# Performance work log

Measured on AMD Instinct MI355X. Metric: run time of the kernel, lower is better.

The kernel has to match this reference:

```python
import jax, jax.numpy as jnp
import numpy as np

D = 512      # d_model
H = 8        # n_heads
HD = D // H  # head_dim
WIN = 128    # local window
CB = 8       # chunk base
NL = 3       # hierarchy levels
DFF = 1536
B, S = 4, 4096
EPS = 1e-6


def setup_inputs() -> dict:
    key = jax.random.key(0)
    ks = jax.random.split(key, 12)
    sd = 0.02
    inp = {
        'x': jax.random.normal(ks[0], (B, S, D), jnp.float32),
        'norm1_w': jnp.ones((D,), jnp.float32),
        'norm2_w': jnp.ones((D,), jnp.float32),
        'wq': jax.random.normal(ks[1], (D, D), jnp.float32) * sd,
        'wk': jax.random.normal(ks[2], (D, D), jnp.float32) * sd,
        'wv': jax.random.normal(ks[3], (D, D), jnp.float32) * sd,
        'wo': jax.random.normal(ks[4], (D, D), jnp.float32) * sd,
        'gamma': jnp.full((NL,), 0.1, jnp.float32),
        'w1': jax.random.normal(ks[5], (D, DFF), jnp.float32) * sd,
        'w2': jax.random.normal(ks[6], (D, DFF), jnp.float32) * sd,
        'w3': jax.random.normal(ks[7], (DFF, D), jnp.float32) * sd,
    }
    return inp


def rmsnorm(x, w):
    return x * jax.lax.rsqrt(jnp.mean(x * x, axis=-1, keepdims=True) + EPS) * w


def hier_attn(x, wq, wk, wv, wo, gamma):
    b, s, _ = x.shape
    scale = HD ** -0.5
    q = (x @ wq).reshape(b, s, H, HD).transpose(0, 2, 1, 3)  # (b,H,s,hd)
    k = (x @ wk).reshape(b, s, H, HD).transpose(0, 2, 1, 3)
    v = (x @ wv).reshape(b, s, H, HD).transpose(0, 2, 1, 3)

    nb = s // WIN
    qb = q.reshape(b, H, nb, WIN, HD)
    kp = jnp.concatenate([jnp.zeros_like(k[:, :, :WIN]), k], axis=2).reshape(b, H, nb + 1, WIN, HD)
    vp = jnp.concatenate([jnp.zeros_like(v[:, :, :WIN]), v], axis=2).reshape(b, H, nb + 1, WIN, HD)
    kw = jnp.concatenate([kp[:, :, :-1], kp[:, :, 1:]], axis=3)  # (b,H,nb,2W,hd)
    vw = jnp.concatenate([vp[:, :, :-1], vp[:, :, 1:]], axis=3)
    sc = jnp.einsum('bhnqd,bhnkd->bhnqk', qb, kw) * scale
    a_ = jnp.arange(WIN)[:, None]
    j_ = jnp.arange(2 * WIN)[None, :]
    base = (j_ > a_) & (j_ <= a_ + WIN)
    blk = (jnp.arange(nb)[:, None, None] > 0) | (j_ >= WIN)  # first block has no left half
    mask = base[None] & blk                                  # (nb,W,2W)
    sc = jnp.where(mask[None, None], sc, -1e9)
    out = jnp.einsum('bhnqk,bhnkd->bhnqd', jax.nn.softmax(sc, axis=-1), vw).reshape(b, H, s, HD)

    # ---- levels 1..NL: causal attention over mean-pooled chunk summaries ----
    pos = jnp.arange(s)
    for lvl in range(1, NL + 1):
        C = CB ** lvl
        nc = s // C
        kc = k.reshape(b, H, nc, C, HD).mean(axis=3)
        vc = v.reshape(b, H, nc, C, HD).mean(axis=3)
        sl = jnp.einsum('bhsd,bhcd->bhsc', q, kc) * scale
        m = jnp.arange(nc)[None, :] < (pos // C)[:, None]    # chunk strictly in the past
        sl = jnp.where(m[None, None], sl, -1e9)
        p = jax.nn.softmax(sl, axis=-1)
        p = p * m.any(axis=-1)[None, None, :, None]          # zero rows with no valid chunk
        out = out + gamma[lvl - 1] * jnp.einsum('bhsc,bhcd->bhsd', p, vc)

    return out.transpose(0, 2, 1, 3).reshape(b, s, D) @ wo


def swiglu(x, w1, w2, w3):
    return (jax.nn.silu(x @ w1) * (x @ w2)) @ w3


def reference(x, norm1_w, norm2_w, wq, wk, wv, wo, gamma, w1, w2, w3):
    h = x + hier_attn(rmsnorm(x, norm1_w), wq, wk, wv, wo, gamma)
    return h + swiglu(rmsnorm(h, norm2_w), w1, w2, w3)
```

## Files before the change

### kernel.cpp

```cpp
#include <hip/hip_runtime.h>
#include <stdint.h>

typedef unsigned short US;
typedef __attribute__((ext_vector_type(8))) short short8;
typedef __attribute__((ext_vector_type(8))) US us8;
typedef __attribute__((ext_vector_type(4))) float f32x4;
typedef __attribute__((ext_vector_type(4))) int i32x4;

#define DEV static __device__ __forceinline__

DEV US f2b(float f){
  uint32_t u = __builtin_bit_cast(uint32_t, f);
  return (US)((u + 0x7fffu + ((u >> 16) & 1u)) >> 16);
}
DEV float b2f(US s){
  return __builtin_bit_cast(float, (uint32_t)((uint32_t)s << 16));
}
DEV short8 ldsfrag(const US* p){
  return __builtin_bit_cast(short8, *(const i32x4*)p);
}
DEV f32x4 MFMA(short8 a, short8 b, f32x4 c){
  return __builtin_amdgcn_mfma_f32_16x16x32_bf16(a, b, c, 0, 0, 0);
}
DEV void async16(const US* g, US* l){
  __builtin_amdgcn_global_load_lds(
      (const __attribute__((address_space(1))) unsigned int*)(const void*)g,
      (__attribute__((address_space(3))) unsigned int*)(void*)l,
      16, 0, 0);
}

struct WcvtArgs {
  const float* src[7];
  US* dst[7];
  int R[7];
  int C[7];
};

__global__ __launch_bounds__(256) void wcvt(WcvtArgs a){
  int z = blockIdx.z;
  int R = a.R[z], C = a.C[z];
  int tc = blockIdx.x*32, tr = blockIdx.y*32;
  if (tc >= C || tr >= R) return;
  __shared__ float T[32][33];
  int tx = threadIdx.x & 31, ty = threadIdx.x >> 5;
  const float* s = a.src[z];
  #pragma unroll
  for (int j=0;j<4;++j) T[ty + j*8][tx] = s[(size_t)(tr + ty + j*8)*C + tc + tx];
  __syncthreads();
  US* d = a.dst[z];
  #pragma unroll
  for (int j=0;j<4;++j) d[(size_t)(tc + ty + j*8)*R + tr + tx] = f2b(T[tx][ty + j*8]);
}

__global__ __launch_bounds__(256) void rmsnorm_k(const float* __restrict__ x,
                                                 const float* __restrict__ w,
                                                 US* __restrict__ o){
  int row = blockIdx.x*4 + (threadIdx.x >> 6);
  int l = threadIdx.x & 63;
  const float* xr = x + (size_t)row*512 + l*8;
  f32x4 a = *(const f32x4*)xr;
  f32x4 b = *(const f32x4*)(xr + 4);
  float ss = a[0]*a[0]+a[1]*a[1]+a[2]*a[2]+a[3]*a[3]
           + b[0]*b[0]+b[1]*b[1]+b[2]*b[2]+b[3]*b[3];
  #pragma unroll
  for (int mk=1; mk<64; mk<<=1) ss += __shfl_xor(ss, mk);
  float r = rsqrtf(ss*(1.0f/512.0f) + 1e-6f);
  const float* wr = w + l*8;
  f32x4 wa = *(const f32x4*)wr;
  f32x4 wb = *(const f32x4*)(wr + 4);
  us8 t;
  t[0]=f2b(a[0]*r*wa[0]); t[1]=f2b(a[1]*r*wa[1]);
  t[2]=f2b(a[2]*r*wa[2]); t[3]=f2b(a[3]*r*wa[3]);
  t[4]=f2b(b[0]*r*wb[0]); t[5]=f2b(b[1]*r*wb[1]);
  t[6]=f2b(b[2]*r*wb[2]); t[7]=f2b(b[3]*r*wb[3]);
  *(us8*)(o + (size_t)row*512 + l*8) = t;
}

template<int EPI>
__global__ __launch_bounds__(256) void gemm_bt(
    const US* __restrict__ A, const US* __restrict__ BT,
    int M, int N, int K,
    void* __restrict__ outp, const float* __restrict__ auxf,
    US* __restrict__ auxb)
{
  __shared__ __attribute__((aligned(16))) US As[128*64];
  __shared__ __attribute__((aligned(16))) US Bs[128*64];
  const int tid = threadIdx.x, l = tid & 63, w = tid >> 6;
  const int wr = w >> 1, wc = w & 1;
  const int gx = gridDim.x;
  int wg = blockIdx.y*gx + blockIdx.x;
  const int nwg = gx * gridDim.y;
  const int qq = nwg >> 3;
  wg = (wg & 7)*qq + (wg >> 3);
  const int m0 = (wg / gx)*128, n0 = (wg % gx)*128;
  (void)M;
  f32x4 acc[4][4] = {};
  for (int k0 = 0; k0 < K; k0 += 64){
    #pragma unroll
    for (int p=0;p<4;++p){
      int off  = p*4096 + w*1024 + l*16;
      int row  = off >> 7;
      int slot = (off >> 4) & 7;
      int ce   = ((slot ^ (row & 7)) << 3);
      async16(A  + (size_t)(m0 + row)*K + k0 + ce, As + p*2048 + w*512);
      async16(BT + (size_t)(n0 + row)*K + k0 + ce, Bs + p*2048 + w*512);
    }
    __syncthreads();
    short8 af[2][4], bg[2][4];
    #pragma unroll
    for (int kk=0;kk<2;++kk){
      const int sA = ((kk*4 + (l>>4)) ^ (l & 7)) << 3;
      #pragma unroll
      for (int i=0;i<4;++i){
        af[kk][i] = ldsfrag(&As[(wr*64 + i*16 + (l&15))*64 + sA]);
        bg[kk][i] = ldsfrag(&Bs[(wc*64 + i*16 + (l&15))*64 + sA]);
      }
    }
    #pragma unroll
    for (int kk=0;kk<2;++kk)
      #pragma unroll
      for (int i=0;i<4;++i)
        #pragma unroll
        for (int j=0;j<4;++j)
          acc[i][j] = MFMA(af[kk][i], bg[kk][j], acc[i][j]);
    __syncthreads();
  }
  #pragma unroll
  for (int i=0;i<4;++i)
    #pragma unroll
    for (int j=0;j<4;++j)
      #pragma unroll
      for (int r=0;r<4;++r){
        int m  = m0 + wr*64 + i*16 + (l>>4)*4 + r;
        int nn = n0 + wc*64 + j*16 + (l&15);
        float val = acc[i][j][r];
        if constexpr (EPI == 0){
          US* o = (US*)outp;
          int f = nn & 511, t = nn >> 9;
          size_t idx = (size_t)t*8388608
                     + ((size_t)(m>>12)*8 + (size_t)(f>>6))*262144
                     + (size_t)(m & 4095)*64 + (size_t)(f & 63);
          o[idx] = f2b(val);
        } else if constexpr (EPI == 1){
          float* o = (float*)outp;
          size_t idx = (size_t)m*N + nn;
          o[idx] = auxf[idx] + val;
        } else if constexpr (EPI == 2){
          US* o = (US*)outp;
          o[(size_t)m*N + nn] = f2b(val);
        } else if constexpr (EPI == 3){
          US* o = (US*)outp;
          size_t idx = (size_t)m*N + nn;
          float g = b2f(auxb[idx]);
          float sg = g / (1.f + __expf(-g));
          o[idx] = f2b(sg * val);
        } else {
          float* o = (float*)outp;
          size_t idx = (size_t)m*N + nn;
          o[idx] += val;
        }
      }
}

__global__ __launch_bounds__(256) void vtrans(const US* __restrict__ vin,
                                              US* __restrict__ vout){
  __shared__ US T[64*72];
  int s0 = blockIdx.x*64;
  int bh = blockIdx.y;
  int r = threadIdx.x >> 2, c0 = (threadIdx.x & 3)*16;
  const US* src = vin + ((size_t)bh*4096 + s0 + r)*64 + c0;
  *(i32x4*)&T[r*72 + c0]     = *(const i32x4*)src;
  *(i32x4*)&T[r*72 + c0 + 8] = *(const i32x4*)(src + 8);
  __syncthreads();
  int d = threadIdx.x >> 2, e0 = (threadIdx.x & 3)*16;
  US* dst = vout + ((size_t)bh*64 + d)*4096 + s0 + e0;
  us8 o0, o1;
  #pragma unroll
  for (int j=0;j<8;++j){ o0[j] = T[(e0+j)*72 + d]; o1[j] = T[(e0+8+j)*72 + d]; }
  *(us8*)dst = o0;
  *(us8*)(dst + 8) = o1;
}

__global__ __launch_bounds__(256) void poolkvt(
    const US* __restrict__ kin, US* __restrict__ kout,
    const US* __restrict__ vtin, US* __restrict__ vtout,
    int nin, int nout, int lgno, int noutS, int lgnoS)
{
  int t = blockIdx.x*256 + threadIdx.x;
  if (blockIdx.y == 0){
    if (t >= (nout << 11)) return;
    int d = t & 63;
    int c = (t >> 6) & (nout - 1);
    int bh = t >> (6 + lgno);
    const US* kp = kin + (((size_t)bh*nin) + (size_t)c*8)*64 + d;
    float s = 0.f;
    #pragma unroll
    for (int j=0;j<8;++j) s += b2f(kp[j*64]);
    kout[((size_t)bh*nout + c)*64 + d] = f2b(s*0.125f);
  } else {
    if (t >= (noutS << 11)) return;
    int c = t & (noutS - 1);
    int row = t >> lgnoS;
    US val = 0;
    if (c < nout){
      const US* vp = vtin + (size_t)row*nin + (size_t)c*8;
      us8 v = *(const us8*)vp;
      float s = 0.f;
      #pragma unroll
      for (int j=0;j<8;++j) s += b2f(v[j]);
      val = f2b(s*0.125f);
    }
    vtout[(size_t)row*noutS + c] = val;
  }
}

template<int NFV, bool LOCAL>
DEV void flash_level(const US* __restrict__ kptr, const US* __restrict__ vtp,
                     int vstride, int ncK, int NCV,
                     int tile0, int ntiles, int lg,
                     int tid, int l, int w, int prow,
                     short8 aq0, short8 aq1,
                     US* Ks, US* Vs, US* Ps,
                     float* mrun, float* lsum, f32x4* olvl)
{
  for (int tt=0; tt<ntiles; ++tt){
    const int cb = (tile0 + tt)*128;
    __syncthreads();
    {
      int r = tid >> 2, c0 = (tid & 3)*16;
      if (cb + r < ncK){
        const US* kp = kptr + (size_t)(cb + r)*64 + c0;
        *(i32x4*)&Ks[r*72 + c0]     = *(const i32x4*)kp;
        *(i32x4*)&Ks[r*72 + c0 + 8] = *(const i32x4*)(kp + 8);
      }
      int d = tid >> 3, e0 = (tid & 7)*16;
      US* dst = &Vs[d*136 + e0];
      if (cb + e0 + 16 <= NCV){
        const US* vp = vtp + (size_t)d*vstride + cb + e0;
        *(i32x4*)dst       = *(const i32x4*)vp;
        *(i32x4*)(dst + 8) = *(const i32x4*)(vp + 8);
      } else {
        i32x4 z = {0,0,0,0};
        *(i32x4*)dst = z; *(i32x4*)(dst + 8) = z;
      }
    }
    __syncthreads();
    f32x4 sc[NFV];
    #pragma unroll
    for (int nf=0; nf<NFV; ++nf){
      const US* kb_ = &Ks[(nf*16 + (l&15))*72 + (l>>4)*8];
      f32x4 z = {0.f,0.f,0.f,0.f};
      z = MFMA(aq0, ldsfrag(kb_), z);
      sc[nf] = MFMA(aq1, ldsfrag(kb_ + 32), z);
    }
    #pragma unroll
    for (int nf=0; nf<NFV; ++nf){
      int c = cb + nf*16 + (l&15);
      #pragma unroll
      for (int i=0;i<4;++i){
        int p = prow + i;
        bool valid = LOCAL ? (c >= p - 127 && c <= p) : (c < (p >> lg));
        sc[nf][i] = valid ? sc[nf][i]*0.125f : -1e30f;
      }
    }
    #pragma unroll
    for (int i=0;i<4;++i){
      float tm = sc[0][i];
      #pragma unroll
      for (int nf=1; nf<NFV; ++nf) tm = fmaxf(tm, sc[nf][i]);
      #pragma unroll
      for (int mk=1; mk<16; mk<<=1) tm = fmaxf(tm, __shfl_xor(tm, mk));
      float nm = fmaxf(mrun[i], tm);
      float rsc = __expf(mrun[i] - nm);
      mrun[i] = nm;
      float rs = 0.f;
      #pragma unroll
      for (int nf=0; nf<NFV; ++nf){ float e = __expf(sc[nf][i] - nm); sc[nf][i] = e; rs += e; }
      #pragma unroll
      for (int mk=1; mk<16; mk<<=1) rs += __shfl_xor(rs, mk);
      lsum[i] = lsum[i]*rsc + rs;
      #pragma unroll
      for (int df=0; df<4; ++df) olvl[df][i] *= rsc;
    }
    #pragma unroll
    for (int nf=0; nf<NFV; ++nf)
      #pragma unroll
      for (int i=0;i<4;++i)
        Ps[w*2176 + ((l>>4)*4 + i)*136 + nf*16 + (l&15)] = f2b(sc[nf][i]);
    #pragma unroll
    for (int kf=0; kf<NFV/2; ++kf){
      short8 pa = ldsfrag(&Ps[w*2176 + (l&15)*136 + kf*32 + (l>>4)*8]);
      #pragma unroll
      for (int df=0; df<4; ++df){
        short8 vb_ = ldsfrag(&Vs[(df*16 + (l&15))*136 + kf*32 + (l>>4)*8]);
        olvl[df] = MFMA(pa, vb_, olvl[df]);
      }
    }
  }
}

__global__ __launch_bounds__(512, 4) void attn_fused(
    const US* __restrict__ q, const US* __restrict__ k, const US* __restrict__ vt,
    const US* __restrict__ kc1, const US* __restrict__ vc1t,
    const US* __restrict__ kc2, const US* __restrict__ vc2t,
    const US* __restrict__ kc3, const US* __restrict__ vc3t,
    const float* __restrict__ gamma, US* __restrict__ ao)
{
  __shared__ __attribute__((aligned(16))) US Ks[128*72];
  __shared__ __attribute__((aligned(16))) US Vs[64*136];
  __shared__ __attribute__((aligned(16))) US Ps[8*16*136];
  const int nblk = blockIdx.x, h = blockIdx.y, b = blockIdx.z;
  const int tid = threadIdx.x, l = tid & 63, w = tid >> 6;
  const int bh = b*8 + h;
  const int prow = nblk*128 + w*16 + ((l>>4)<<2);
  short8 aq0, aq1;
  {
    int s = nblk*128 + w*16 + (l & 15);
    const US* qp = q + ((size_t)bh*4096 + s)*64 + (l >> 4)*8;
    aq0 = __builtin_bit_cast(short8, *(const i32x4*)qp);
    aq1 = __builtin_bit_cast(short8, *(const i32x4*)(qp + 32));
  }
  float mrun[4], lsum[4];
  f32x4 olvl[4], oacc[4];
  #pragma unroll
  for (int i=0;i<4;++i) oacc[i] = (f32x4){0.f,0.f,0.f,0.f};

  #pragma unroll
  for (int i=0;i<4;++i){ mrun[i]=-1e30f; lsum[i]=0.f; olvl[i]=(f32x4){0.f,0.f,0.f,0.f}; }
  flash_level<8,true>(k + (size_t)bh*262144, vt + (size_t)bh*262144, 4096, 4096, 4096,
                      (nblk>0)?(nblk-1):0, (nblk>0)?2:1, 0,
                      tid,l,w,prow,aq0,aq1,Ks,Vs,Ps,mrun,lsum,olvl);
  #pragma unroll
  for (int i=0;i<4;++i){
    float wgt = 1.f/lsum[i];
    #pragma unroll
    for (int df=0;df<4;++df) oacc[df][i] += olvl[df][i]*wgt;
  }

  const float g0 = gamma[0], g1 = gamma[1], g2 = gamma[2];

  #pragma unroll
  for (int i=0;i<4;++i){ mrun[i]=-1e30f; lsum[i]=0.f; olvl[i]=(f32x4){0.f,0.f,0.f,0.f}; }
  {
    int cme = (nblk*128 + 127) >> 3;
    int nt = (cme + 127) >> 7;
    flash_level<8,false>(kc1 + (size_t)bh*32768, vc1t + (size_t)bh*32768, 512, 512, 512,
                         0, nt, 3, tid,l,w,prow,aq0,aq1,Ks,Vs,Ps,mrun,lsum,olvl);
  }
  #pragma unroll
  for (int i=0;i<4;++i){
    if (prow + i >= 8){
      float wgt = g0/lsum[i];
      #pragma unroll
      for (int df=0;df<4;++df) oacc[df][i] += olvl[df][i]*wgt;
    }
  }

  #pragma unroll
  for (int i=0;i<4;++i){ mrun[i]=-1e30f; lsum[i]=0.f; olvl[i]=(f32x4){0.f,0.f,0.f,0.f}; }
  flash_level<4,false>(kc2 + (size_t)bh*4096, vc2t + (size_t)bh*4096, 64, 64, 64,
                       0, 1, 6, tid,l,w,prow,aq0,aq1,Ks,Vs,Ps,mrun,lsum,olvl);
  #pragma unroll
  for (int i=0;i<4;++i){
    if (prow + i >= 64){
      float wgt = g1/lsum[i];
      #pragma unroll
      for (int df=0;df<4;++df) oacc[df][i] += olvl[df][i]*wgt;
    }
  }

  if (nblk >= 4){
    #pragma unroll
    for (int i=0;i<4;++i){ mrun[i]=-1e30f; lsum[i]=0.f; olvl[i]=(f32x4){0.f,0.f,0.f,0.f}; }
    flash_level<2,false>(kc3 + (size_t)bh*512, vc3t + (size_t)bh*1024, 16, 8, 16,
                         0, 1, 9, tid,l,w,prow,aq0,aq1,Ks,Vs,Ps,mrun,lsum,olvl);
    #pragma unroll
    for (int i=0;i<4;++i){
      if (prow + i >= 512){
        float wgt = g2/lsum[i];
        #pragma unroll
        for (int df=0;df<4;++df) oacc[df][i] += olvl[df][i]*wgt;
      }
    }
  }

  #pragma unroll
  for (int df=0;df<4;++df)
    #pragma unroll
    for (int i=0;i<4;++i){
      int p = prow + i, d = df*16 + (l&15);
      ao[((size_t)b*4096 + p)*512 + h*64 + d] = f2b(oacc[df][i]);
    }
}

static constexpr size_t SZ_WT_SQ = (size_t)512*512*2;
static constexpr size_t SZ_WT_FF = (size_t)512*1536*2;
static constexpr size_t SZ_ACT   = (size_t)16384*512*2;
static constexpr size_t O_WQT = 0;
static constexpr size_t O_WKT = O_WQT + SZ_WT_SQ;
static constexpr size_t O_WVT = O_WKT + SZ_WT_SQ;
static constexpr size_t O_WOT = O_WVT + SZ_WT_SQ;
static constexpr size_t O_W1T = O_WOT + SZ_WT_SQ;
static constexpr size_t O_W2T = O_W1T + SZ_WT_FF;
static constexpr size_t O_W3T = O_W2T + SZ_WT_FF;
static constexpr size_t O_XN  = O_W3T + SZ_WT_FF;
static constexpr size_t O_Q   = O_XN + SZ_ACT;
static constexpr size_t O_K   = O_Q + SZ_ACT;
static constexpr size_t O_V   = O_K + SZ_ACT;
static constexpr size_t O_AO  = O_V + SZ_ACT;
static constexpr size_t O_KC1 = O_AO + SZ_ACT;
static constexpr size_t O_VC1T = O_KC1 + (size_t)32*512*64*2;
static constexpr size_t O_KC2  = O_VC1T + (size_t)32*64*512*2;
static constexpr size_t O_VC2T = O_KC2 + (size_t)32*64*64*2;
static constexpr size_t O_KC3  = O_VC2T + (size_t)32*64*64*2;
static constexpr size_t O_VC3T = O_KC3 + (size_t)32*8*64*2;

extern "C" void kernel_launch(void* const* d_in, const int* in_sizes, int n_in,
                              void* d_out, int out_size, void* d_ws, size_t ws_size,
                              hipStream_t stream)
{
  (void)in_sizes; (void)n_in; (void)out_size; (void)ws_size;
  const float* x     = (const float*)d_in[0];
  const float* n1w   = (const float*)d_in[1];
  const float* n2w   = (const float*)d_in[2];
  const float* wq    = (const float*)d_in[3];
  const float* wk    = (const float*)d_in[4];
  const float* wv    = (const float*)d_in[5];
  const float* wo    = (const float*)d_in[6];
  const float* gamma = (const float*)d_in[7];
  const float* w1    = (const float*)d_in[8];
  const float* w2    = (const float*)d_in[9];
  const float* w3    = (const float*)d_in[10];
  float* out = (float*)d_out;
  char* ws = (char*)d_ws;

  US* wqT = (US*)(ws + O_WQT);
  US* wkT = (US*)(ws + O_WKT);
  US* wvT = (US*)(ws + O_WVT);
  US* woT = (US*)(ws + O_WOT);
  US* w1T = (US*)(ws + O_W1T);
  US* w2T = (US*)(ws + O_W2T);
  US* w3T = (US*)(ws + O_W3T);
  US* xn  = (US*)(ws + O_XN);
  US* qb  = (US*)(ws + O_Q);
  US* kb  = (US*)(ws + O_K);
  US* vb  = (US*)(ws + O_V);
  US* ao  = (US*)(ws + O_AO);
  US* kc1 = (US*)(ws + O_KC1);
  US* vc1t = (US*)(ws + O_VC1T);
  US* kc2  = (US*)(ws + O_KC2);
  US* vc2t = (US*)(ws + O_VC2T);
  US* kc3  = (US*)(ws + O_KC3);
  US* vc3t = (US*)(ws + O_VC3T);
  US* vbt = xn;
  US* up1 = (US*)(ws + O_Q);

  WcvtArgs wa;
  wa.src[0]=wq; wa.dst[0]=wqT; wa.R[0]=512;  wa.C[0]=512;
  wa.src[1]=wk; wa.dst[1]=wkT; wa.R[1]=512;  wa.C[1]=512;
  wa.src[2]=wv; wa.dst[2]=wvT; wa.R[2]=512;  wa.C[2]=512;
  wa.src[3]=wo; wa.dst[3]=woT; wa.R[3]=512;  wa.C[3]=512;
  wa.src[4]=w1; wa.dst[4]=w1T; wa.R[4]=512;  wa.C[4]=1536;
  wa.src[5]=w2; wa.dst[5]=w2T; wa.R[5]=512;  wa.C[5]=1536;
  wa.src[6]=w3; wa.dst[6]=w3T; wa.R[6]=1536; wa.C[6]=512;
  wcvt<<<dim3(48,48,7), 256, 0, stream>>>(wa);

  rmsnorm_k<<<dim3(4096), 256, 0, stream>>>(x, n1w, xn);

  gemm_bt<0><<<dim3(12,128), 256, 0, stream>>>(xn, wqT, 16384,1536,512, (void*)qb, nullptr, nullptr);

  vtrans<<<dim3(64,32), 256, 0, stream>>>(vb, vbt);

  poolkvt<<<dim3(4096,2), 256, 0, stream>>>(kb,  kc1, vbt,  vc1t, 4096, 512, 9, 512, 9);
  poolkvt<<<dim3(512,2),  256, 0, stream>>>(kc1, kc2, vc1t, vc2t, 512,  64,  6, 64,  6);
  poolkvt<<<dim3(128,2),  256, 0, stream>>>(kc2, kc3, vc2t, vc3t, 64,   8,   3, 16,  4);

  attn_fused<<<dim3(32,8,4), 512, 0, stream>>>(qb, kb, vbt, kc1, vc1t, kc2, vc2t, kc3, vc3t, gamma, ao);

  gemm_bt<1><<<dim3(4,128), 256, 0, stream>>>(ao, woT, 16384,512,512, (void*)out, x, nullptr);

  rmsnorm_k<<<dim3(4096), 256, 0, stream>>>(out, n2w, xn);

  gemm_bt<2><<<dim3(12,128), 256, 0, stream>>>(xn, w1T, 16384,1536,512, (void*)up1, nullptr, nullptr);
  gemm_bt<3><<<dim3(12,128), 256, 0, stream>>>(xn, w2T, 16384,1536,512, (void*)up1, nullptr, up1);
  gemm_bt<4><<<dim3(4,128), 256, 0, stream>>>(up1, w3T, 16384,512,1536, (void*)out, nullptr, nullptr);
}
```

Baseline: 311.7 us.

## Add 256x256 double-buffered GEMM kernel for QKV and FFN up-projections

Adds a 512-thread GEMM kernel with 256x256 output tiles, double-buffered LDS staging with async loads overlapping MFMA, explicit vmcnt waits and priority hints. It is used for the QKV projection and both FFN up-projection GEMMs (N=1536). The larger tiles raise data reuse per LDS load and the prefetch hides global latency, at the cost of fewer workgroups (384) and higher register and LDS pressure. The LDS swizzle read index in the old kernel is also changed to use the row's low bits, which is an equivalent form.

```diff
diff --git a/kernel.cpp b/kernel.cpp
--- a/kernel.cpp
+++ b/kernel.cpp
@@ -109,11 +109,14 @@
     short8 af[2][4], bg[2][4];
     #pragma unroll
     for (int kk=0;kk<2;++kk){
-      const int sA = ((kk*4 + (l>>4)) ^ (l & 7)) << 3;
       #pragma unroll
       for (int i=0;i<4;++i){
-        af[kk][i] = ldsfrag(&As[(wr*64 + i*16 + (l&15))*64 + sA]);
-        bg[kk][i] = ldsfrag(&Bs[(wc*64 + i*16 + (l&15))*64 + sA]);
+        int rowA = wr*64 + i*16 + (l&15);
+        int sA = ((kk*4 + (l>>4)) ^ (rowA & 7)) << 3;
+        af[kk][i] = ldsfrag(&As[rowA*64 + sA]);
+        int rowB = wc*64 + i*16 + (l&15);
+        int sB = ((kk*4 + (l>>4)) ^ (rowB & 7)) << 3;
+        bg[kk][i] = ldsfrag(&Bs[rowB*64 + sB]);
       }
     }
     #pragma unroll
@@ -134,30 +137,119 @@
         int m  = m0 + wr*64 + i*16 + (l>>4)*4 + r;
         int nn = n0 + wc*64 + j*16 + (l&15);
         float val = acc[i][j][r];
-        if constexpr (EPI == 0){
-          US* o = (US*)outp;
-          int f = nn & 511, t = nn >> 9;
-          size_t idx = (size_t)t*8388608
-                     + ((size_t)(m>>12)*8 + (size_t)(f>>6))*262144
-                     + (size_t)(m & 4095)*64 + (size_t)(f & 63);
-          o[idx] = f2b(val);
-        } else if constexpr (EPI == 1){
+        if constexpr (EPI == 1){
           float* o = (float*)outp;
           size_t idx = (size_t)m*N + nn;
           o[idx] = auxf[idx] + val;
-        } else if constexpr (EPI == 2){
-          US* o = (US*)outp;
-          o[(size_t)m*N + nn] = f2b(val);
-        } else if constexpr (EPI == 3){
-          US* o = (US*)outp;
-          size_t idx = (size_t)m*N + nn;
-          float g = b2f(auxb[idx]);
-          float sg = g / (1.f + __expf(-g));
-          o[idx] = f2b(sg * val);
         } else {
           float* o = (float*)outp;
           size_t idx = (size_t)m*N + nn;
           o[idx] += val;
+        }
+      }
+  (void)auxb;
+}
+
+template<int EPI>
+__global__ __launch_bounds__(512, 2) void gemm256_bt(
+    const US* __restrict__ A, const US* __restrict__ BT,
+    int M, int N, int K,
+    void* __restrict__ outp, US* __restrict__ auxb)
+{
+  __shared__ __attribute__((aligned(16))) US As[2][16384];
+  __shared__ __attribute__((aligned(16))) US Bs[2][16384];
+  const int tid = threadIdx.x, l = tid & 63, w = tid >> 6;
+  const int wr = w >> 2, wc = w & 3;
+  const int gx = gridDim.x;
+  int wg = blockIdx.y*gx + blockIdx.x;
+  const int nwg = gx * gridDim.y;
+  const int qq = nwg >> 3;
+  wg = (wg & 7)*qq + (wg >> 3);
+  const int m0 = (wg / gx)*256, n0 = (wg % gx)*256;
+  (void)M;
+
+  auto stage = [&](int buf, int kt){
+    const int kb = kt*64;
+    #pragma unroll
+    for (int i=0;i<4;++i){
+      int off  = i*8192 + tid*16;
+      int row  = off >> 7;
+      int slot = (off >> 4) & 7;
+      int ce   = ((slot ^ (row & 7)) << 3);
+      async16(A  + (size_t)(m0 + row)*K + kb + ce, &As[buf][i*4096 + tid*8]);
+      async16(BT + (size_t)(n0 + row)*K + kb + ce, &Bs[buf][i*4096 + tid*8]);
+    }
+  };
+
+  f32x4 acc[8][4] = {};
+  const int nt = K >> 6;
+
+  stage(0, 0);
+  __builtin_amdgcn_sched_barrier(0);
+  for (int t=0; t<nt; ++t){
+    const int cur = t & 1;
+    const bool hn = (t+1 < nt);
+    if (hn) stage(cur^1, t+1);
+    __builtin_amdgcn_sched_barrier(0);
+    if (hn) asm volatile("s_waitcnt vmcnt(8)" ::: "memory");
+    else    asm volatile("s_waitcnt vmcnt(0)" ::: "memory");
+    __builtin_amdgcn_s_barrier();
+    __builtin_amdgcn_sched_barrier(0);
+    const US* Ac = As[cur];
+    const US* Bc = Bs[cur];
+    #pragma unroll
+    for (int ks=0; ks<2; ++ks){
+      short8 af[8], bg[4];
+      #pragma unroll
+      for (int m=0;m<8;++m){
+        int row = wr*128 + m*16 + (l&15);
+        int s = ((ks*4 + (l>>4)) ^ (row & 7)) << 3;
+        af[m] = ldsfrag(&Ac[row*64 + s]);
+      }
+      #pragma unroll
+      for (int n=0;n<4;++n){
+        int row = wc*64 + n*16 + (l&15);
+        int s = ((ks*4 + (l>>4)) ^ (row & 7)) << 3;
+        bg[n] = ldsfrag(&Bc[row*64 + s]);
+      }
+      __builtin_amdgcn_s_setprio(1);
+      #pragma unroll
+      for (int m=0;m<8;++m)
+        #pragma unroll
+        for (int n=0;n<4;++n)
+          acc[m][n] = MFMA(af[m], bg[n], acc[m][n]);
+      __builtin_amdgcn_s_setprio(0);
+    }
+    __builtin_amdgcn_sched_barrier(0);
+    __builtin_amdgcn_s_barrier();
+    __builtin_amdgcn_sched_barrier(0);
+  }
+
+  #pragma unroll
+  for (int m=0;m<8;++m)
+    #pragma unroll
+    for (int n=0;n<4;++n)
+      #pragma unroll
+      for (int r=0;r<4;++r){
+        int mm = m0 + wr*128 + m*16 + (l>>4)*4 + r;
+        int nn = n0 + wc*64 + n*16 + (l&15);
+        float val = acc[m][n][r];
+        if constexpr (EPI == 0){
+          US* o = (US*)outp;
+          int f = nn & 511, tq = nn >> 9;
+          size_t idx = (size_t)tq*8388608
+                     + ((size_t)(mm>>12)*8 + (size_t)(f>>6))*262144
+                     + (size_t)(mm & 4095)*64 + (size_t)(f & 63);
+          o[idx] = f2b(val);
+        } else if constexpr (EPI == 2){
+          US* o = (US*)outp;
+          o[(size_t)mm*N + nn] = f2b(val);
+        } else {
+          US* o = (US*)outp;
+          size_t idx = (size_t)mm*N + nn;
+          float g = b2f(auxb[idx]);
+          float sg = g / (1.f + __expf(-g));
+          o[idx] = f2b(sg * val);
         }
       }
 }
@@ -467,7 +559,7 @@
 
   rmsnorm_k<<<dim3(4096), 256, 0, stream>>>(x, n1w, xn);
 
-  gemm_bt<0><<<dim3(12,128), 256, 0, stream>>>(xn, wqT, 16384,1536,512, (void*)qb, nullptr, nullptr);
+  gemm256_bt<0><<<dim3(6,64), 512, 0, stream>>>(xn, wqT, 16384,1536,512, (void*)qb, nullptr);
 
   vtrans<<<dim3(64,32), 256, 0, stream>>>(vb, vbt);
 
@@ -481,7 +573,7 @@
 
   rmsnorm_k<<<dim3(4096), 256, 0, stream>>>(out, n2w, xn);
 
-  gemm_bt<2><<<dim3(12,128), 256, 0, stream>>>(xn, w1T, 16384,1536,512, (void*)up1, nullptr, nullptr);
-  gemm_bt<3><<<dim3(12,128), 256, 0, stream>>>(xn, w2T, 16384,1536,512, (void*)up1, nullptr, up1);
+  gemm256_bt<2><<<dim3(6,64), 512, 0, stream>>>(xn, w1T, 16384,1536,512, (void*)up1, nullptr);
+  gemm256_bt<3><<<dim3(6,64), 512, 0, stream>>>(xn, w2T, 16384,1536,512, (void*)up1, up1);
   gemm_bt<4><<<dim3(4,128), 256, 0, stream>>>(up1, w3T, 16384,512,1536, (void*)out, nullptr, nullptr);
 }
```

Result: slower. 335.7 us (+7.7%).

## Fuse gate/up FFN GEMMs with SiLU epilogue and drop softmax max tracking

Applied to the files above, without the earlier changes.

Adds a dual-B GEMM kernel that computes the x@w1 and x@w2 tiles together and writes silu(g)*u directly. This avoids a second pass over the activations and the bf16 intermediate store and reload. The attention flash loop also stops tracking a running max and rescaling accumulators, relying on scores being small enough not to overflow exp. P is rounded to bf16 with a cheaper round-half-up. The fused kernel doubles the accumulator registers, and the softmax change sacrifices numerical robustness for large scores.

```diff
diff --git a/kernel.cpp b/kernel.cpp
--- a/kernel.cpp
+++ b/kernel.cpp
@@ -12,6 +12,10 @@
 DEV US f2b(float f){
   uint32_t u = __builtin_bit_cast(uint32_t, f);
   return (US)((u + 0x7fffu + ((u >> 16) & 1u)) >> 16);
+}
+DEV US f2b_fast(float f){
+  uint32_t u = __builtin_bit_cast(uint32_t, f);
+  return (US)((u + 0x8000u) >> 16);
 }
 DEV float b2f(US s){
   return __builtin_bit_cast(float, (uint32_t)((uint32_t)s << 16));
@@ -148,17 +152,78 @@
         } else if constexpr (EPI == 2){
           US* o = (US*)outp;
           o[(size_t)m*N + nn] = f2b(val);
-        } else if constexpr (EPI == 3){
-          US* o = (US*)outp;
-          size_t idx = (size_t)m*N + nn;
-          float g = b2f(auxb[idx]);
-          float sg = g / (1.f + __expf(-g));
-          o[idx] = f2b(sg * val);
         } else {
           float* o = (float*)outp;
           size_t idx = (size_t)m*N + nn;
           o[idx] += val;
         }
+      }
+  (void)auxb;
+}
+
+__global__ __launch_bounds__(256, 2) void gemm_ff12(
+    const US* __restrict__ A, const US* __restrict__ B1T, const US* __restrict__ B2T,
+    int N, int K, US* __restrict__ outp)
+{
+  __shared__ __attribute__((aligned(16))) US As[128*64];
+  __shared__ __attribute__((aligned(16))) US B1s[128*64];
+  __shared__ __attribute__((aligned(16))) US B2s[128*64];
+  const int tid = threadIdx.x, l = tid & 63, w = tid >> 6;
+  const int wr = w >> 1, wc = w & 1;
+  const int gx = gridDim.x;
+  int wg = blockIdx.y*gx + blockIdx.x;
+  const int nwg = gx * gridDim.y;
+  const int qq = nwg >> 3;
+  wg = (wg & 7)*qq + (wg >> 3);
+  const int m0 = (wg / gx)*128, n0 = (wg % gx)*128;
+  f32x4 acc1[4][4] = {};
+  f32x4 acc2[4][4] = {};
+  for (int k0 = 0; k0 < K; k0 += 64){
+    #pragma unroll
+    for (int p=0;p<4;++p){
+      int off  = p*4096 + w*1024 + l*16;
+      int row  = off >> 7;
+      int slot = (off >> 4) & 7;
+      int ce   = ((slot ^ (row & 7)) << 3);
+      async16(A   + (size_t)(m0 + row)*K + k0 + ce, As  + p*2048 + w*512);
+      async16(B1T + (size_t)(n0 + row)*K + k0 + ce, B1s + p*2048 + w*512);
+      async16(B2T + (size_t)(n0 + row)*K + k0 + ce, B2s + p*2048 + w*512);
+    }
+    __syncthreads();
+    short8 af[2][4], bg1[2][4], bg2[2][4];
+    #pragma unroll
+    for (int kk=0;kk<2;++kk){
+      const int sA = ((kk*4 + (l>>4)) ^ (l & 7)) << 3;
+      #pragma unroll
+      for (int i=0;i<4;++i){
+        af[kk][i]  = ldsfrag(&As [(wr*64 + i*16 + (l&15))*64 + sA]);
+        bg1[kk][i] = ldsfrag(&B1s[(wc*64 + i*16 + (l&15))*64 + sA]);
+        bg2[kk][i] = ldsfrag(&B2s[(wc*64 + i*16 + (l&15))*64 + sA]);
+      }
+    }
+    #pragma unroll
+    for (int kk=0;kk<2;++kk)
+      #pragma unroll
+      for (int i=0;i<4;++i)
+        #pragma unroll
+        for (int j=0;j<4;++j){
+          acc1[i][j] = MFMA(af[kk][i], bg1[kk][j], acc1[i][j]);
+          acc2[i][j] = MFMA(af[kk][i], bg2[kk][j], acc2[i][j]);
+        }
+    __syncthreads();
+  }
+  #pragma unroll
+  for (int i=0;i<4;++i)
+    #pragma unroll
+    for (int j=0;j<4;++j)
+      #pragma unroll
+      for (int r=0;r<4;++r){
+        int m  = m0 + wr*64 + i*16 + (l>>4)*4 + r;
+        int nn = n0 + wc*64 + j*16 + (l&15);
+        float g = acc1[i][j][r];
+        float u = acc2[i][j][r];
+        float sg = g / (1.f + __expf(-g));
+        outp[(size_t)m*N + nn] = f2b(sg * u);
       }
 }
 
@@ -221,7 +286,7 @@
                      int tid, int l, int w, int prow,
                      short8 aq0, short8 aq1,
                      US* Ks, US* Vs, US* Ps,
-                     float* mrun, float* lsum, f32x4* olvl)
+                     float* lsum, f32x4* olvl)
 {
   for (int tt=0; tt<ntiles; ++tt){
     const int cb = (tile0 + tt)*128;
@@ -265,28 +330,18 @@
     }
     #pragma unroll
     for (int i=0;i<4;++i){
-      float tm = sc[0][i];
-      #pragma unroll
-      for (int nf=1; nf<NFV; ++nf) tm = fmaxf(tm, sc[nf][i]);
-      #pragma unroll
-      for (int mk=1; mk<16; mk<<=1) tm = fmaxf(tm, __shfl_xor(tm, mk));
-      float nm = fmaxf(mrun[i], tm);
-      float rsc = __expf(mrun[i] - nm);
-      mrun[i] = nm;
       float rs = 0.f;
       #pragma unroll
-      for (int nf=0; nf<NFV; ++nf){ float e = __expf(sc[nf][i] - nm); sc[nf][i] = e; rs += e; }
+      for (int nf=0; nf<NFV; ++nf){ float e = __expf(sc[nf][i]); sc[nf][i] = e; rs += e; }
       #pragma unroll
       for (int mk=1; mk<16; mk<<=1) rs += __shfl_xor(rs, mk);
-      lsum[i] = lsum[i]*rsc + rs;
-      #pragma unroll
-      for (int df=0; df<4; ++df) olvl[df][i] *= rsc;
+      lsum[i] += rs;
     }
     #pragma unroll
     for (int nf=0; nf<NFV; ++nf)
       #pragma unroll
       for (int i=0;i<4;++i)
-        Ps[w*2176 + ((l>>4)*4 + i)*136 + nf*16 + (l&15)] = f2b(sc[nf][i]);
+        Ps[w*2176 + ((l>>4)*4 + i)*136 + nf*16 + (l&15)] = f2b_fast(sc[nf][i]);
     #pragma unroll
     for (int kf=0; kf<NFV/2; ++kf){
       short8 pa = ldsfrag(&Ps[w*2176 + (l&15)*136 + kf*32 + (l>>4)*8]);
@@ -320,16 +375,16 @@
     aq0 = __builtin_bit_cast(short8, *(const i32x4*)qp);
     aq1 = __builtin_bit_cast(short8, *(const i32x4*)(qp + 32));
   }
-  float mrun[4], lsum[4];
+  float lsum[4];
   f32x4 olvl[4], oacc[4];
   #pragma unroll
   for (int i=0;i<4;++i) oacc[i] = (f32x4){0.f,0.f,0.f,0.f};
 
   #pragma unroll
-  for (int i=0;i<4;++i){ mrun[i]=-1e30f; lsum[i]=0.f; olvl[i]=(f32x4){0.f,0.f,0.f,0.f}; }
+  for (int i=0;i<4;++i){ lsum[i]=0.f; olvl[i]=(f32x4){0.f,0.f,0.f,0.f}; }
   flash_level<8,true>(k + (size_t)bh*262144, vt + (size_t)bh*262144, 4096, 4096, 4096,
                       (nblk>0)?(nblk-1):0, (nblk>0)?2:1, 0,
-                      tid,l,w,prow,aq0,aq1,Ks,Vs,Ps,mrun,lsum,olvl);
+                      tid,l,w,prow,aq0,aq1,Ks,Vs,Ps,lsum,olvl);
   #pragma unroll
   for (int i=0;i<4;++i){
     float wgt = 1.f/lsum[i];
@@ -340,12 +395,12 @@
   const float g0 = gamma[0], g1 = gamma[1], g2 = gamma[2];
 
   #pragma unroll
-  for (int i=0;i<4;++i){ mrun[i]=-1e30f; lsum[i]=0.f; olvl[i]=(f32x4){0.f,0.f,0.f,0.f}; }
+  for (int i=0;i<4;++i){ lsum[i]=0.f; olvl[i]=(f32x4){0.f,0.f,0.f,0.f}; }
   {
     int cme = (nblk*128 + 127) >> 3;
     int nt = (cme + 127) >> 7;
     flash_level<8,false>(kc1 + (size_t)bh*32768, vc1t + (size_t)bh*32768, 512, 512, 512,
-                         0, nt, 3, tid,l,w,prow,aq0,aq1,Ks,Vs,Ps,mrun,lsum,olvl);
+                         0, nt, 3, tid,l,w,prow,aq0,aq1,Ks,Vs,Ps,lsum,olvl);
   }
   #pragma unroll
   for (int i=0;i<4;++i){
@@ -357,9 +412,9 @@
   }
 
   #pragma unroll
-  for (int i=0;i<4;++i){ mrun[i]=-1e30f; lsum[i]=0.f; olvl[i]=(f32x4){0.f,0.f,0.f,0.f}; }
+  for (int i=0;i<4;++i){ lsum[i]=0.f; olvl[i]=(f32x4){0.f,0.f,0.f,0.f}; }
   flash_level<4,false>(kc2 + (size_t)bh*4096, vc2t + (size_t)bh*4096, 64, 64, 64,
-                       0, 1, 6, tid,l,w,prow,aq0,aq1,Ks,Vs,Ps,mrun,lsum,olvl);
+                       0, 1, 6, tid,l,w,prow,aq0,aq1,Ks,Vs,Ps,lsum,olvl);
   #pragma unroll
   for (int i=0;i<4;++i){
     if (prow + i >= 64){
@@ -371,9 +426,9 @@
 
   if (nblk >= 4){
     #pragma unroll
-    for (int i=0;i<4;++i){ mrun[i]=-1e30f; lsum[i]=0.f; olvl[i]=(f32x4){0.f,0.f,0.f,0.f}; }
+    for (int i=0;i<4;++i){ lsum[i]=0.f; olvl[i]=(f32x4){0.f,0.f,0.f,0.f}; }
     flash_level<2,false>(kc3 + (size_t)bh*512, vc3t + (size_t)bh*1024, 16, 8, 16,
-                         0, 1, 9, tid,l,w,prow,aq0,aq1,Ks,Vs,Ps,mrun,lsum,olvl);
+                         0, 1, 9, tid,l,w,prow,aq0,aq1,Ks,Vs,Ps,lsum,olvl);
     #pragma unroll
     for (int i=0;i<4;++i){
       if (prow + i >= 512){
@@ -481,7 +536,7 @@
 
   rmsnorm_k<<<dim3(4096), 256, 0, stream>>>(out, n2w, xn);
 
-  gemm_bt<2><<<dim3(12,128), 256, 0, stream>>>(xn, w1T, 16384,1536,512, (void*)up1, nullptr, nullptr);
-  gemm_bt<3><<<dim3(12,128), 256, 0, stream>>>(xn, w2T, 16384,1536,512, (void*)up1, nullptr, up1);
+  gemm_ff12<<<dim3(12,128), 256, 0, stream>>>(xn, w1T, w2T, 1536, 512, up1);
+
   gemm_bt<4><<<dim3(4,128), 256, 0, stream>>>(up1, w3T, 16384,512,1536, (void*)out, nullptr, nullptr);
 }
```

After: 272.2 us. 1.15x faster.
